# Kernel tuning notes

Measured on AMD Instinct MI355X. Metric: run time of the kernel, lower is better.

## Reference

```python
import jax, jax.numpy as jnp
import numpy as np

B, T, L, H = 16, 16, 512, 768


def setup_inputs() -> dict:
    key = jax.random.key(0)
    k1, k2, k3, k4, k5, k6 = jax.random.split(key, 6)
    hn = jax.random.normal(k1, (B, L, H), dtype=jnp.float32)
    decoder_out = jax.random.normal(k2, (B, L, H), dtype=jnp.float32)
    W1 = jax.random.normal(k3, (H, H), dtype=jnp.float32) * (1.0 / np.sqrt(H))
    W2 = jax.random.normal(k4, (H, H), dtype=jnp.float32) * (1.0 / np.sqrt(H))
    V = jax.random.normal(k5, (H,), dtype=jnp.float32) * (1.0 / np.sqrt(H))
    # Ragged, consistent pointer indices: T monotone segment starts per sample,
    # gold boundary Yindex[b,t] in [Xindex[b,t], L).
    step = L // T  # 32
    Xindex = jnp.broadcast_to(jnp.arange(T, dtype=jnp.int64) * step, (B, T))
    offsets = jax.random.randint(k6, (B, T), 0, step, dtype=jnp.int64)
    Yindex = Xindex + offsets
    lens = jnp.full((B,), L, dtype=jnp.int64)
    return {"hn": hn, "decoder_out": decoder_out, "W1": W1, "W2": W2, "V": V,
            "Xindex": Xindex, "Yindex": Yindex, "lens": lens}


def reference(hn, decoder_out, W1, W2, V, Xindex, Yindex, lens):
    # Faithful batched form of training_decoder + pointerLayer:
    #   for each sample i, step j:
    #     en = hn[i, Xindex[i,j]:lens[i]]            (ragged suffix)
    #     dj = decoder_out[i, Yindex[i,j]]           (cur_dj = decoder_out[cur_groundy])
    #     s  = selu(V @ selu(W1 en + W2 dj))
    #     loss += NLL(log_softmax(s), Yindex[i,j]-Xindex[i,j])
    WE = jnp.einsum('blh,gh->blg', hn, W1)                        # [B,L,H]  nnW1(en)
    dj = jnp.take_along_axis(decoder_out, Yindex[:, :, None], axis=1)  # [B,T,H]
    WD = jnp.einsum('bth,gh->btg', dj, W2)                        # [B,T,H]  nnW2(dj)
    act = jax.nn.selu(WE[:, None, :, :] + WD[:, :, None, :])      # [B,T,L,H]
    scores = jax.nn.selu(jnp.einsum('btlh,h->btl', act, V))       # [B,T,L]
    pos = jnp.arange(hn.shape[1])
    mask = (pos[None, None, :] >= Xindex[:, :, None]) & (pos[None, None, :] < lens[:, None, None])
    neg_inf = jnp.finfo(scores.dtype).min
    masked = jnp.where(mask, scores, neg_inf)
    logp = masked - jax.scipy.special.logsumexp(masked, axis=-1, keepdims=True)
    # logits index (Yindex - Xindex) in the sliced array == global index Yindex
    gold = jnp.take_along_axis(logp, Yindex[:, :, None], axis=-1)[..., 0]  # [B,T]
    return -jnp.mean(gold)
```

## Files before the change

### kernel.cpp

```cpp
#include <hip/hip_runtime.h>
#include <hip/hip_bf16.h>
#include <math.h>

#define SELU_SCALE 1.0507009873554805f
#define SELU_ALPHA 1.6732632423543772f

static constexpr int B_ = 16, T_ = 16, L_ = 512, H_ = 768;
static constexpr int WSZ = 768 * 768;
static constexpr int HNELEM = B_ * L_ * H_;
static constexpr int DJELEM = B_ * T_ * H_;
static constexpr int ALLELEM = HNELEM + 2 * WSZ + DJELEM;

typedef __bf16 bf16x8 __attribute__((ext_vector_type(8)));
typedef float  f32x4  __attribute__((ext_vector_type(4)));

__device__ __forceinline__ float bf_lo(unsigned u) { return __uint_as_float(u << 16); }
__device__ __forceinline__ float bf_hi(unsigned u) { return __uint_as_float(u & 0xFFFF0000u); }

__device__ __forceinline__ float selu_core(float x) {
    float e = fmaf(__expf(x), SELU_ALPHA, -SELU_ALPHA);
    return x > 0.0f ? x : e;
}

__device__ __forceinline__ bf16x8 pack8(float4 a, float4 b) {
    bf16x8 o;
    o[0] = (__bf16)a.x; o[1] = (__bf16)a.y; o[2] = (__bf16)a.z; o[3] = (__bf16)a.w;
    o[4] = (__bf16)b.x; o[5] = (__bf16)b.y; o[6] = (__bf16)b.z; o[7] = (__bf16)b.w;
    return o;
}

__global__ __launch_bounds__(256) void prep_k(
        const float* __restrict__ hn, const float* __restrict__ dec,
        const float* __restrict__ w1, const float* __restrict__ w2,
        const int* __restrict__ Yi,
        __bf16* __restrict__ allb, float* __restrict__ out) {
    if (blockIdx.x == 0 && threadIdx.x == 0) out[0] = 0.0f;
    int idx = (blockIdx.x * 256 + threadIdx.x) * 8;
    const float* src;
    if (idx < HNELEM) {
        src = hn + idx;
    } else if (idx < HNELEM + WSZ) {
        src = w1 + (idx - HNELEM);
    } else if (idx < HNELEM + 2 * WSZ) {
        src = w2 + (idx - HNELEM - WSZ);
    } else {
        int e = idx - (HNELEM + 2 * WSZ);
        int r = e / 768, c = e - r * 768;
        src = dec + ((size_t)((r >> 4) * L_ + Yi[r])) * H_ + c;
    }
    float4 a = *(const float4*)src;
    float4 b = *(const float4*)(src + 4);
    *(bf16x8*)(allb + idx) = pack8(a, b);
}

__global__ __launch_bounds__(256, 2) void gemm_k(
        const __bf16* __restrict__ allb,
        __bf16* __restrict__ web, float* __restrict__ wdf) {
    int bx = blockIdx.x;
    const __bf16 *Ab, *Bb; int m0, n0; bool wd;
    if (bx < 384) {
        wd = false; Ab = allb; Bb = allb + HNELEM;
        m0 = (bx & 63) * 128; n0 = (bx >> 6) * 128;
    } else {
        wd = true; bx -= 384; Ab = allb + HNELEM + 2 * WSZ; Bb = allb + HNELEM + WSZ;
        m0 = (bx & 1) * 128;  n0 = (bx >> 1) * 128;
    }

    const int tid = threadIdx.x, wave = tid >> 6, lane = tid & 63;
    const int wm = (wave >> 1) * 64, wn = (wave & 1) * 64;
    const int lr = lane & 15, q = lane >> 4;

    const __bf16* pA[4]; const __bf16* pB[4];
#pragma unroll
    for (int i = 0; i < 4; ++i) pA[i] = Ab + (size_t)(m0 + wm + i * 16 + lr) * 768 + q * 8;
#pragma unroll
    for (int j = 0; j < 4; ++j) pB[j] = Bb + (size_t)(n0 + wn + j * 16 + lr) * 768 + q * 8;

    f32x4 acc[4][4] = {};
    bf16x8 a0v[4], b0v[4], a1v[4], b1v[4], a2v[4], b2v[4];

#pragma unroll
    for (int i = 0; i < 4; ++i) { a0v[i] = *(const bf16x8*)(pA[i]);      b0v[i] = *(const bf16x8*)(pB[i]); }
#pragma unroll
    for (int i = 0; i < 4; ++i) { a1v[i] = *(const bf16x8*)(pA[i] + 32); b1v[i] = *(const bf16x8*)(pB[i] + 32); }

#define PHASE(SA, SB, LA, LB, KL)                                              \
    {                                                                          \
        if ((KL) < 768) {                                                      \
            _Pragma("unroll")                                                  \
            for (int i = 0; i < 4; ++i) {                                      \
                LA[i] = *(const bf16x8*)(pA[i] + (KL));                        \
                LB[i] = *(const bf16x8*)(pB[i] + (KL));                        \
            }                                                                  \
        }                                                                      \
        _Pragma("unroll")                                                      \
        for (int i = 0; i < 4; ++i)                                            \
            _Pragma("unroll")                                                  \
            for (int j = 0; j < 4; ++j)                                        \
                acc[i][j] = __builtin_amdgcn_mfma_f32_16x16x32_bf16(           \
                    SA[i], SB[j], acc[i][j], 0, 0, 0);                         \
    }

#pragma unroll 1
    for (int k0 = 0; k0 < 768; k0 += 96) {
        PHASE(a0v, b0v, a2v, b2v, k0 + 64)
        PHASE(a1v, b1v, a0v, b0v, k0 + 96)
        PHASE(a2v, b2v, a1v, b1v, k0 + 128)
    }
#undef PHASE

#pragma unroll
    for (int i = 0; i < 4; ++i)
#pragma unroll
        for (int j = 0; j < 4; ++j)
#pragma unroll
            for (int r = 0; r < 4; ++r) {
                int row = m0 + wm + i * 16 + q * 4 + r;
                int col = n0 + wn + j * 16 + lr;
                if (!wd) web[(size_t)row * 768 + col] = (__bf16)acc[i][j][r];
                else     wdf[(size_t)row * 768 + col] = acc[i][j][r];
            }
}

__global__ __launch_bounds__(256, 4) void scores_k(
        const __bf16* __restrict__ web, const float* __restrict__ wdf,
        const float* __restrict__ V, const int* __restrict__ Xi,
        float* __restrict__ scores) {
    const int b  = blockIdx.x;
    const int l0 = ((int)gridDim.y - 1 - (int)blockIdx.y) * 16;
    const int t0 = blockIdx.z * 8;
    const int tid = threadIdx.x;
    const int ls = tid >> 4, hc = tid & 15;
    const int l  = l0 + ls;
    const int h0 = hc * 8;

    float we[48], vv[48];
    const __bf16* wr = web + ((size_t)(b * L_ + l)) * H_ + h0;
#pragma unroll
    for (int j = 0; j < 6; ++j) {
        uint4 u = *(const uint4*)(wr + j * 128);
        we[j*8+0] = bf_lo(u.x); we[j*8+1] = bf_hi(u.x);
        we[j*8+2] = bf_lo(u.y); we[j*8+3] = bf_hi(u.y);
        we[j*8+4] = bf_lo(u.z); we[j*8+5] = bf_hi(u.z);
        we[j*8+6] = bf_lo(u.w); we[j*8+7] = bf_hi(u.w);
    }
    const float* vp = V + h0;
#pragma unroll
    for (int j = 0; j < 6; ++j) {
        float4 a = *(const float4*)(vp + j * 128);
        float4 c = *(const float4*)(vp + j * 128 + 4);
        vv[j*8+0] = a.x; vv[j*8+1] = a.y; vv[j*8+2] = a.z; vv[j*8+3] = a.w;
        vv[j*8+4] = c.x; vv[j*8+5] = c.y; vv[j*8+6] = c.z; vv[j*8+7] = c.w;
    }

    const int wmaxl = l0 + ((tid >> 6) << 2) + 3;
    const int bT = b * T_;
#pragma unroll 1
    for (int t = t0; t < t0 + 8; ++t) {
        const int X = Xi[bT + t];
        if (wmaxl < X) continue;
        const float* wdp = wdf + ((size_t)(bT + t)) * H_ + h0;
        float a0 = 0.f, a1 = 0.f, a2 = 0.f, a3 = 0.f;
#pragma unroll
        for (int j = 0; j < 6; ++j) {
            float4 x = *(const float4*)(wdp + j * 128);
            float4 y = *(const float4*)(wdp + j * 128 + 4);
            a0 = fmaf(selu_core(we[j*8+0] + x.x), vv[j*8+0], a0);
            a1 = fmaf(selu_core(we[j*8+1] + x.y), vv[j*8+1], a1);
            a2 = fmaf(selu_core(we[j*8+2] + x.z), vv[j*8+2], a2);
            a3 = fmaf(selu_core(we[j*8+3] + x.w), vv[j*8+3], a3);
            a0 = fmaf(selu_core(we[j*8+4] + y.x), vv[j*8+4], a0);
            a1 = fmaf(selu_core(we[j*8+5] + y.y), vv[j*8+5], a1);
            a2 = fmaf(selu_core(we[j*8+6] + y.z), vv[j*8+6], a2);
            a3 = fmaf(selu_core(we[j*8+7] + y.w), vv[j*8+7], a3);
        }
        float dot = (a0 + a1) + (a2 + a3);
        dot += __shfl_xor(dot, 1);
        dot += __shfl_xor(dot, 2);
        dot += __shfl_xor(dot, 4);
        dot += __shfl_xor(dot, 8);
        if (hc == 0) {
            dot *= SELU_SCALE;
            float sc = dot > 0.0f ? SELU_SCALE * dot
                                  : SELU_SCALE * SELU_ALPHA * (__expf(dot) - 1.0f);
            scores[((size_t)(bT + t)) * L_ + l] = sc;
        }
    }
}

__global__ __launch_bounds__(64) void loss_k(
        const float* __restrict__ scores, const int* __restrict__ Xi,
        const int* __restrict__ Yi, float* __restrict__ out) {
    const int bt = blockIdx.x;
    const int lane = threadIdx.x;
    const int X = Xi[bt];
    const int Y = Yi[bt];
    const float* row = scores + (size_t)bt * L_;

    float m = -INFINITY;
    for (int l = X + lane; l < L_; l += 64) m = fmaxf(m, row[l]);
#pragma unroll
    for (int off = 32; off > 0; off >>= 1) m = fmaxf(m, __shfl_xor(m, off));

    float s = 0.0f;
    for (int l = X + lane; l < L_; l += 64) s += __expf(row[l] - m);
#pragma unroll
    for (int off = 32; off > 0; off >>= 1) s += __shfl_xor(s, off);

    if (lane == 0)
        atomicAdd(out, (m + __logf(s) - row[Y]) * (1.0f / (B_ * T_)));
}

extern "C" void kernel_launch(void* const* d_in, const int* in_sizes, int n_in,
                              void* d_out, int out_size, void* d_ws, size_t ws_size,
                              hipStream_t stream) {
    const float* hn  = (const float*)d_in[0];
    const float* dec = (const float*)d_in[1];
    const float* W1  = (const float*)d_in[2];
    const float* W2  = (const float*)d_in[3];
    const float* V   = (const float*)d_in[4];
    const int*   Xi  = (const int*)d_in[5];
    const int*   Yi  = (const int*)d_in[6];
    float* out = (float*)d_out;

    char* ws = (char*)d_ws;
    size_t off = 0;
    auto alloc = [&](size_t bytes) -> char* {
        char* p = ws + off;
        off += (bytes + 255) & ~(size_t)255;
        return p;
    };
    __bf16* web    = (__bf16*)alloc((size_t)B_ * L_ * H_ * 2);
    float*  wdf    = (float*)alloc((size_t)B_ * T_ * H_ * 4);
    float*  scores = (float*)alloc((size_t)B_ * T_ * L_ * 4);
    __bf16* allb   = (__bf16*)alloc((size_t)ALLELEM * 2);

    prep_k<<<ALLELEM / (256 * 8), 256, 0, stream>>>(hn, dec, W1, W2, Yi, allb, out);
    gemm_k<<<396, 256, 0, stream>>>(allb, web, wdf);
    scores_k<<<dim3(B_, L_ / 16, 2), 256, 0, stream>>>(web, wdf, V, Xi, scores);
    loss_k<<<B_ * T_, 64, 0, stream>>>(scores, Xi, Yi, out);
}
```

Baseline: 176.8 us.

## Retile GEMM to 128x32 tiles with full-K B panel staged in LDS

Restructures the projection GEMM from 128x128 register-only tiles into 128x32 tiles, raising the grid from 396 to 1584 blocks. Each block stages its entire 32x768 slice of the weight matrix into padded shared memory, and each wave computes a 32x32 sub-tile with a 4-deep register prefetch ring. The block-index mapping groups 8 consecutive M tiles per N tile for cache locality, and launch bounds rise to 3 waves per EU. This aims to fill more CUs and improve occupancy. In exchange each block reuses less of the A operand, so total global reads of hn grow.

Result: faster. 172.7 us (-2.3%).

```diff
diff --git a/kernel.cpp b/kernel.cpp
--- a/kernel.cpp
+++ b/kernel.cpp
@@ -53,70 +53,90 @@
     *(bf16x8*)(allb + idx) = pack8(a, b);
 }
 
-__global__ __launch_bounds__(256, 2) void gemm_k(
+__global__ __launch_bounds__(256, 3) void gemm_k(
         const __bf16* __restrict__ allb,
         __bf16* __restrict__ web, float* __restrict__ wdf) {
+    __shared__ __bf16 Bs[32][776];
+
     int bx = blockIdx.x;
     const __bf16 *Ab, *Bb; int m0, n0; bool wd;
-    if (bx < 384) {
+    if (bx < 1536) {
         wd = false; Ab = allb; Bb = allb + HNELEM;
-        m0 = (bx & 63) * 128; n0 = (bx >> 6) * 128;
+        int c8 = bx & 7, rest = bx >> 3;
+        n0 = (rest % 24) * 32;
+        m0 = (c8 + (rest / 24) * 8) * 128;
     } else {
-        wd = true; bx -= 384; Ab = allb + HNELEM + 2 * WSZ; Bb = allb + HNELEM + WSZ;
-        m0 = (bx & 1) * 128;  n0 = (bx >> 1) * 128;
+        wd = true; int b2 = bx - 1536;
+        Ab = allb + HNELEM + 2 * WSZ; Bb = allb + HNELEM + WSZ;
+        m0 = (b2 & 1) * 128; n0 = (b2 >> 1) * 32;
     }
 
     const int tid = threadIdx.x, wave = tid >> 6, lane = tid & 63;
-    const int wm = (wave >> 1) * 64, wn = (wave & 1) * 64;
     const int lr = lane & 15, q = lane >> 4;
 
-    const __bf16* pA[4]; const __bf16* pB[4];
-#pragma unroll
-    for (int i = 0; i < 4; ++i) pA[i] = Ab + (size_t)(m0 + wm + i * 16 + lr) * 768 + q * 8;
-#pragma unroll
-    for (int j = 0; j < 4; ++j) pB[j] = Bb + (size_t)(n0 + wn + j * 16 + lr) * 768 + q * 8;
-
-    f32x4 acc[4][4] = {};
-    bf16x8 a0v[4], b0v[4], a1v[4], b1v[4], a2v[4], b2v[4];
-
-#pragma unroll
-    for (int i = 0; i < 4; ++i) { a0v[i] = *(const bf16x8*)(pA[i]);      b0v[i] = *(const bf16x8*)(pB[i]); }
-#pragma unroll
-    for (int i = 0; i < 4; ++i) { a1v[i] = *(const bf16x8*)(pA[i] + 32); b1v[i] = *(const bf16x8*)(pB[i] + 32); }
-
-#define PHASE(SA, SB, LA, LB, KL)                                              \
-    {                                                                          \
-        if ((KL) < 768) {                                                      \
-            _Pragma("unroll")                                                  \
-            for (int i = 0; i < 4; ++i) {                                      \
-                LA[i] = *(const bf16x8*)(pA[i] + (KL));                        \
-                LB[i] = *(const bf16x8*)(pB[i] + (KL));                        \
-            }                                                                  \
-        }                                                                      \
-        _Pragma("unroll")                                                      \
-        for (int i = 0; i < 4; ++i)                                            \
-            _Pragma("unroll")                                                  \
-            for (int j = 0; j < 4; ++j)                                        \
-                acc[i][j] = __builtin_amdgcn_mfma_f32_16x16x32_bf16(           \
-                    SA[i], SB[j], acc[i][j], 0, 0, 0);                         \
+    {
+        int row = tid >> 3, k0 = (tid & 7) * 8;
+        const __bf16* src = Bb + (size_t)(n0 + row) * 768 + k0;
+        __bf16* dst = &Bs[row][k0];
+#pragma unroll
+        for (int s = 0; s < 12; ++s)
+            *(bf16x8*)(dst + s * 64) = *(const bf16x8*)(src + s * 64);
+    }
+
+    const __bf16* pA0 = Ab + (size_t)(m0 + wave * 32 + lr) * 768 + q * 8;
+    const __bf16* pA1 = pA0 + (size_t)16 * 768;
+    const __bf16* pB0 = &Bs[lr][q * 8];
+    const __bf16* pB1 = &Bs[16 + lr][q * 8];
+
+    f32x4 acc[2][2] = {};
+    bf16x8 a0s[4], a1s[4], b0s[4], b1s[4];
+
+#pragma unroll
+    for (int s = 0; s < 4; ++s) {
+        a0s[s] = *(const bf16x8*)(pA0 + s * 32);
+        a1s[s] = *(const bf16x8*)(pA1 + s * 32);
+    }
+    __syncthreads();
+#pragma unroll
+    for (int s = 0; s < 4; ++s) {
+        b0s[s] = *(const bf16x8*)(pB0 + s * 32);
+        b1s[s] = *(const bf16x8*)(pB1 + s * 32);
+    }
+
+#define MM(s)                                                                   \
+    acc[0][0] = __builtin_amdgcn_mfma_f32_16x16x32_bf16(a0s[s], b0s[s], acc[0][0], 0, 0, 0); \
+    acc[0][1] = __builtin_amdgcn_mfma_f32_16x16x32_bf16(a0s[s], b1s[s], acc[0][1], 0, 0, 0); \
+    acc[1][0] = __builtin_amdgcn_mfma_f32_16x16x32_bf16(a1s[s], b0s[s], acc[1][0], 0, 0, 0); \
+    acc[1][1] = __builtin_amdgcn_mfma_f32_16x16x32_bf16(a1s[s], b1s[s], acc[1][1], 0, 0, 0);
+
+#define STEP(s, c)                                                              \
+    {                                                                           \
+        MM(s)                                                                   \
+        a0s[s] = *(const bf16x8*)(pA0 + ((c) + 4) * 32);                        \
+        a1s[s] = *(const bf16x8*)(pA1 + ((c) + 4) * 32);                        \
+        b0s[s] = *(const bf16x8*)(pB0 + ((c) + 4) * 32);                        \
+        b1s[s] = *(const bf16x8*)(pB1 + ((c) + 4) * 32);                        \
     }
 
 #pragma unroll 1
-    for (int k0 = 0; k0 < 768; k0 += 96) {
-        PHASE(a0v, b0v, a2v, b2v, k0 + 64)
-        PHASE(a1v, b1v, a0v, b0v, k0 + 96)
-        PHASE(a2v, b2v, a1v, b1v, k0 + 128)
-    }
-#undef PHASE
-
-#pragma unroll
-    for (int i = 0; i < 4; ++i)
-#pragma unroll
-        for (int j = 0; j < 4; ++j)
+    for (int c = 0; c < 20; c += 4) {
+        STEP(0, c)
+        STEP(1, c + 1)
+        STEP(2, c + 2)
+        STEP(3, c + 3)
+    }
+    MM(0) MM(1) MM(2) MM(3)
+#undef STEP
+#undef MM
+
+#pragma unroll
+    for (int i = 0; i < 2; ++i)
+#pragma unroll
+        for (int j = 0; j < 2; ++j)
 #pragma unroll
             for (int r = 0; r < 4; ++r) {
-                int row = m0 + wm + i * 16 + q * 4 + r;
-                int col = n0 + wn + j * 16 + lr;
+                int row = m0 + wave * 32 + i * 16 + q * 4 + r;
+                int col = n0 + j * 16 + lr;
                 if (!wd) web[(size_t)row * 768 + col] = (__bf16)acc[i][j][r];
                 else     wdf[(size_t)row * 768 + col] = acc[i][j][r];
             }
@@ -236,7 +256,7 @@
     __bf16* allb   = (__bf16*)alloc((size_t)ALLELEM * 2);
 
     prep_k<<<ALLELEM / (256 * 8), 256, 0, stream>>>(hn, dec, W1, W2, Yi, allb, out);
-    gemm_k<<<396, 256, 0, stream>>>(allb, web, wdf);
+    gemm_k<<<1536 + 48, 256, 0, stream>>>(allb, web, wdf);
     scores_k<<<dim3(B_, L_ / 16, 2), 256, 0, stream>>>(web, wdf, V, Xi, scores);
     loss_k<<<B_ * T_, 64, 0, stream>>>(scores, Xi, Yi, out);
 }
```

## Stage GEMM tiles through LDS with direct global-to-LDS loads and double buffering

Applied to the files above, without the earlier changes.

The GEMM kernel stops having every wave load its own A/B fragments from global memory into registers. Each block now cooperatively stages 128x32 A and B tiles into a double-buffered shared-memory region using global_load_lds, with an XOR swizzle to avoid bank conflicts. Waves then read their fragments from LDS, which cuts redundant global/L2 traffic across the 2x2 wave grid. The cost is a barrier and a full vmcnt(0) wait on every 32-wide k-step, which limits how much load latency is hidden, plus 32KB of LDS per block.

New measurement: 148.9 us. 15.7% less time.

```diff
diff --git a/kernel.cpp b/kernel.cpp
--- a/kernel.cpp
+++ b/kernel.cpp
@@ -21,6 +21,8 @@
     float e = fmaf(__expf(x), SELU_ALPHA, -SELU_ALPHA);
     return x > 0.0f ? x : e;
 }
+
+__device__ __forceinline__ int xsw(int r) { return (r >> 1) & 3; }
 
 __device__ __forceinline__ bf16x8 pack8(float4 a, float4 b) {
     bf16x8 o;
@@ -56,58 +58,79 @@
 __global__ __launch_bounds__(256, 2) void gemm_k(
         const __bf16* __restrict__ allb,
         __bf16* __restrict__ web, float* __restrict__ wdf) {
+    __shared__ __bf16 sm[2][2][4096];
+
     int bx = blockIdx.x;
     const __bf16 *Ab, *Bb; int m0, n0; bool wd;
     if (bx < 384) {
         wd = false; Ab = allb; Bb = allb + HNELEM;
         m0 = (bx & 63) * 128; n0 = (bx >> 6) * 128;
     } else {
-        wd = true; bx -= 384; Ab = allb + HNELEM + 2 * WSZ; Bb = allb + HNELEM + WSZ;
+        wd = true; bx -= 384;
+        Ab = allb + HNELEM + 2 * WSZ; Bb = allb + HNELEM + WSZ;
         m0 = (bx & 1) * 128;  n0 = (bx >> 1) * 128;
     }
 
     const int tid = threadIdx.x, wave = tid >> 6, lane = tid & 63;
     const int wm = (wave >> 1) * 64, wn = (wave & 1) * 64;
     const int lr = lane & 15, q = lane >> 4;
-
-    const __bf16* pA[4]; const __bf16* pB[4];
-#pragma unroll
-    for (int i = 0; i < 4; ++i) pA[i] = Ab + (size_t)(m0 + wm + i * 16 + lr) * 768 + q * 8;
-#pragma unroll
-    for (int j = 0; j < 4; ++j) pB[j] = Bb + (size_t)(n0 + wn + j * 16 + lr) * 768 + q * 8;
+    const int l4 = lane >> 2, sl = lane & 3;
+
+    const int ar0 = wave * 16 + l4, ar1 = ar0 + 64;
+    const __bf16* gA0 = Ab + (size_t)(m0 + ar0) * 768 + (sl ^ xsw(ar0)) * 8;
+    const __bf16* gA1 = Ab + (size_t)(m0 + ar1) * 768 + (sl ^ xsw(ar1)) * 8;
+    const __bf16* gB0 = Bb + (size_t)(n0 + ar0) * 768 + (sl ^ xsw(ar0)) * 8;
+    const __bf16* gB1 = Bb + (size_t)(n0 + ar1) * 768 + (sl ^ xsw(ar1)) * 8;
+    const int ld0 = wave * 512;
+    const int ld1 = 2048 + wave * 512;
+
+    const int aoff0 = (wm + lr) * 32 + (q ^ xsw(wm + lr)) * 8;
+    const int boff0 = (wn + lr) * 32 + (q ^ xsw(wn + lr)) * 8;
 
     f32x4 acc[4][4] = {};
-    bf16x8 a0v[4], b0v[4], a1v[4], b1v[4], a2v[4], b2v[4];
-
-#pragma unroll
-    for (int i = 0; i < 4; ++i) { a0v[i] = *(const bf16x8*)(pA[i]);      b0v[i] = *(const bf16x8*)(pB[i]); }
-#pragma unroll
-    for (int i = 0; i < 4; ++i) { a1v[i] = *(const bf16x8*)(pA[i] + 32); b1v[i] = *(const bf16x8*)(pB[i] + 32); }
-
-#define PHASE(SA, SB, LA, LB, KL)                                              \
-    {                                                                          \
-        if ((KL) < 768) {                                                      \
-            _Pragma("unroll")                                                  \
-            for (int i = 0; i < 4; ++i) {                                      \
-                LA[i] = *(const bf16x8*)(pA[i] + (KL));                        \
-                LB[i] = *(const bf16x8*)(pB[i] + (KL));                        \
-            }                                                                  \
-        }                                                                      \
-        _Pragma("unroll")                                                      \
-        for (int i = 0; i < 4; ++i)                                            \
-            _Pragma("unroll")                                                  \
-            for (int j = 0; j < 4; ++j)                                        \
-                acc[i][j] = __builtin_amdgcn_mfma_f32_16x16x32_bf16(           \
-                    SA[i], SB[j], acc[i][j], 0, 0, 0);                         \
-    }
-
+
+#define STAGE(b, kk)                                                                        \
+    {                                                                                       \
+        __builtin_amdgcn_global_load_lds((const __attribute__((address_space(1))) void*)(gA0 + (kk)), \
+            (__attribute__((address_space(3))) void*)&sm[b][0][ld0], 16, 0, 0);             \
+        __builtin_amdgcn_global_load_lds((const __attribute__((address_space(1))) void*)(gA1 + (kk)), \
+            (__attribute__((address_space(3))) void*)&sm[b][0][ld1], 16, 0, 0);             \
+        __builtin_amdgcn_global_load_lds((const __attribute__((address_space(1))) void*)(gB0 + (kk)), \
+            (__attribute__((address_space(3))) void*)&sm[b][1][ld0], 16, 0, 0);             \
+        __builtin_amdgcn_global_load_lds((const __attribute__((address_space(1))) void*)(gB1 + (kk)), \
+            (__attribute__((address_space(3))) void*)&sm[b][1][ld1], 16, 0, 0);             \
+    }
+
+#define COMPUTE(b)                                                                          \
+    {                                                                                       \
+        bf16x8 af[4], bfr[4];                                                               \
+        _Pragma("unroll")                                                                   \
+        for (int i = 0; i < 4; ++i) af[i]  = *(const bf16x8*)&sm[b][0][aoff0 + i * 512];    \
+        _Pragma("unroll")                                                                   \
+        for (int j = 0; j < 4; ++j) bfr[j] = *(const bf16x8*)&sm[b][1][boff0 + j * 512];    \
+        _Pragma("unroll")                                                                   \
+        for (int i = 0; i < 4; ++i)                                                         \
+            _Pragma("unroll")                                                               \
+            for (int j = 0; j < 4; ++j)                                                     \
+                acc[i][j] = __builtin_amdgcn_mfma_f32_16x16x32_bf16(af[i], bfr[j], acc[i][j], 0, 0, 0); \
+    }
+
+    STAGE(0, 0)
+    asm volatile("s_waitcnt vmcnt(0)" ::: "memory");
+    __builtin_amdgcn_s_barrier();
+
+    int cur = 0;
 #pragma unroll 1
-    for (int k0 = 0; k0 < 768; k0 += 96) {
-        PHASE(a0v, b0v, a2v, b2v, k0 + 64)
-        PHASE(a1v, b1v, a0v, b0v, k0 + 96)
-        PHASE(a2v, b2v, a1v, b1v, k0 + 128)
-    }
-#undef PHASE
+    for (int t = 0; t < 23; ++t) {
+        STAGE(cur ^ 1, (t + 1) * 32)
+        COMPUTE(cur)
+        asm volatile("s_waitcnt vmcnt(0)" ::: "memory");
+        __builtin_amdgcn_s_barrier();
+        cur ^= 1;
+    }
+    COMPUTE(cur)
+#undef STAGE
+#undef COMPUTE
 
 #pragma unroll
     for (int i = 0; i < 4; ++i)
```
